# Kernel optimization log

Hardware: AMD Instinct MI355X
Metric: run time of the kernel (lower is better)

Reference implementation:

```python
import jax, jax.numpy as jnp
import numpy as np

E = 8          # node_emb_dim (number of LSTM ensembles)
H = 128        # fixed_lstm_hidden
D = 8          # feature dim
CONT = 168     # cont_len (encoder length)
HORIZON = 24   # decoder length
T = CONT + HORIZON
B = 4096       # batch of node ids
NUM_TS = 4096


def _lstm(xs, W, U, b, h0, c0):
    """Time-major LSTM (Keras gate order i,f,g,o). xs: [T,B,in]. Returns final (h,c) and all hs."""
    def step(carry, x):
        h, c = carry
        z = x @ W + h @ U + b                      # [B, 4H]
        i, f, g, o = jnp.split(z, 4, axis=-1)
        i = jax.nn.sigmoid(i)
        f = jax.nn.sigmoid(f)
        g = jnp.tanh(g)
        o = jax.nn.sigmoid(o)
        c = f * c + i * g
        h = o * jnp.tanh(c)
        return (h, c), h
    (h, c), hs = jax.lax.scan(step, (h0, c0), xs)
    return h, c, hs


def setup_inputs() -> dict:
    key = jax.random.key(0)
    ks = jax.random.split(key, 12)
    s = 0.05  # small init scale to keep LSTM gates unsaturated
    return {
        "feats": jax.random.normal(ks[0], (T, D), jnp.float32),
        "y_prev": jax.random.normal(ks[1], (CONT, B), jnp.float32),
        "nid": jax.random.randint(ks[2], (B,), 0, NUM_TS, jnp.int32),
        "emb_table": jax.random.uniform(ks[3], (NUM_TS, E), jnp.float32),
        "enc_W": jax.random.normal(ks[4], (E, 1 + D, 4 * H), jnp.float32) * s,
        "enc_U": jax.random.normal(ks[5], (E, H, 4 * H), jnp.float32) * s,
        "enc_b": jnp.zeros((E, 4 * H), jnp.float32),
        "dec_W": jax.random.normal(ks[6], (E, D, 4 * H), jnp.float32) * s,
        "dec_U": jax.random.normal(ks[7], (E, H, 4 * H), jnp.float32) * s,
        "dec_b": jnp.zeros((E, 4 * H), jnp.float32),
        "out_w": jax.random.normal(ks[8], (E, H), jnp.float32) * s,
    }


def reference(feats, y_prev, nid, emb_table, enc_W, enc_U, enc_b, dec_W, dec_U, dec_b, out_w):
    cont_len = y_prev.shape[0]
    b = nid.shape[0]
    # normalized node embedding: abs then row-normalize, then lookup
    embs = jnp.abs(emb_table)
    embs = embs / jnp.sum(embs, axis=1, keepdims=True)
    node_emb = embs[nid]                                   # [B, E]
    # broadcast features over batch (time-major)
    feats_b = jnp.broadcast_to(feats[:, None, :], (feats.shape[0], b, feats.shape[1]))
    enc_inp = jnp.concatenate([y_prev[..., None], feats_b[:cont_len]], axis=-1)  # [CONT,B,1+D]
    feats_futr = feats_b[cont_len:]                        # [HOR,B,D]
    hdim = enc_U.shape[1]
    h0 = jnp.zeros((b, hdim), feats.dtype)
    c0 = jnp.zeros((b, hdim), feats.dtype)

    def run_one(eW, eU, eb, dW, dU, db, ow):
        h, c, _ = _lstm(enc_inp, eW, eU, eb, h0, c0)
        _, _, hs = _lstm(feats_futr, dW, dU, db, h, c)     # [HOR,B,H]
        return jnp.einsum('tbh,h->tb', hs, ow)             # Dense(1, no bias) -> [HOR,B]

    outs = jax.vmap(run_one)(enc_W, enc_U, enc_b, dec_W, dec_U, dec_b, out_w)  # [E,HOR,B]
    fixed_effect = jnp.einsum('etb,be->tb', outs, node_emb)                    # [HOR,B]
    return fixed_effect
```

## Files before the change

### kernel.cpp

```cpp
#include <hip/hip_runtime.h>
#include <stdint.h>
#include <type_traits>

#define NE 8
#define NH 128
#define ND 8
#define NCONT 168
#define NHOR 24
#define NB 4096
#define NG 512
#define BT 64

typedef float f32x4 __attribute__((ext_vector_type(4)));
typedef short bf16x8 __attribute__((ext_vector_type(8)));
typedef unsigned int u32x2 __attribute__((ext_vector_type(2)));

__device__ __forceinline__ unsigned short f2bf(float f){
  union { float f; unsigned u; } v; v.f = f;
  unsigned r = (v.u + 0x7FFFu + ((v.u >> 16) & 1u)) >> 16;
  return (unsigned short)r;
}
__device__ __forceinline__ unsigned cvt_pk_bf16(float lo, float hi){
  unsigned r;
  asm("v_cvt_pk_bf16_f32 %0, %1, %2" : "=v"(r) : "v"(lo), "v"(hi));
  return r;
}
__device__ __forceinline__ float sigm(float x){
  return __builtin_amdgcn_rcpf(1.0f + __builtin_amdgcn_exp2f(-1.44269504f * x));
}
__device__ __forceinline__ float tanh_fast(float x){
  return 1.0f - 2.0f * __builtin_amdgcn_rcpf(1.0f + __builtin_amdgcn_exp2f(2.88539008f * x));
}

__global__ void prep_fxw_enc(const float* __restrict__ feats, const float* __restrict__ W,
                             const float* __restrict__ bias, float* __restrict__ out){
  int idx = blockIdx.x * blockDim.x + threadIdx.x;
  if (idx >= NE * NCONT * NG) return;
  int j = idx & (NG - 1);
  int t = (idx >> 9) % NCONT;
  int e = idx / (NCONT * NG);
  float s = bias[e * NG + j];
  #pragma unroll
  for (int i = 0; i < ND; ++i)
    s += feats[t * ND + i] * W[(e * 9 + 1 + i) * NG + j];
  out[idx] = s;
}

__global__ void prep_fxw_dec(const float* __restrict__ feats, const float* __restrict__ W,
                             const float* __restrict__ bias, float* __restrict__ out){
  int idx = blockIdx.x * blockDim.x + threadIdx.x;
  if (idx >= NE * NHOR * NG) return;
  int j = idx & (NG - 1);
  int t = (idx >> 9) % NHOR;
  int e = idx / (NHOR * NG);
  float s = bias[e * NG + j];
  #pragma unroll
  for (int i = 0; i < ND; ++i)
    s += feats[(NCONT + t) * ND + i] * W[(e * ND + i) * NG + j];
  out[idx] = s;
}

__global__ void prep_node(const int* __restrict__ nid, const float* __restrict__ emb,
                          float* __restrict__ node_w){
  int b = blockIdx.x * blockDim.x + threadIdx.x;
  if (b >= NB) return;
  int n = nid[b];
  float a[NE]; float s = 0.f;
  #pragma unroll
  for (int e = 0; e < NE; ++e){ a[e] = fabsf(emb[n * NE + e]); s += a[e]; }
  float inv = 1.0f / s;
  #pragma unroll
  for (int e = 0; e < NE; ++e) node_w[b * NE + e] = a[e] * inv;
}

__global__ __launch_bounds__(512, 2) void lstm_main(
    const float* __restrict__ y_prev,
    const float* __restrict__ enc_W,
    const float* __restrict__ enc_U,
    const float* __restrict__ dec_U,
    const float* __restrict__ out_w,
    const float* __restrict__ fxw_enc,
    const float* __restrict__ fxw_dec,
    float* __restrict__ ws_out)
{
  __shared__ unsigned short hl[2][BT * NH];
  __shared__ float part[2][BT][9];

  const int tid  = threadIdx.x;
  const int lane = tid & 63;
  const int w    = tid >> 6;
  const int e    = blockIdx.x & 7;
  const int b0   = (blockIdx.x >> 3) * BT;
  const int l15  = lane & 15;
  const int l4   = lane >> 4;
  const int hc0  = w * 16 + l4 * 4;

  const int q   = (l15 >> 2) & 1;
  const int Ae  = l15 * 128 + ((l4 ^ (l15 & 3)) << 3);
  const int rb0 = 2 * (Ae + q * 32);
  const int rb1 = 2 * (Ae + (1 - q) * 32);
  const int wb  = 2 * ((l15 * 128 + hc0) ^ ((l15 & 7) << 3));

  {
    f32x4 z4 = {0.f, 0.f, 0.f, 0.f};
    ((f32x4*)&hl[0][0])[tid]       = z4;
    ((f32x4*)&hl[0][0])[tid + 512] = z4;
  }

  bf16x8 ut[4][4];
  {
    const float* Ub = enc_U + e * NH * NG + w * 16 + l15;
    #pragma unroll
    for (int g = 0; g < 4; ++g)
      #pragma unroll
      for (int kc = 0; kc < 4; ++kc){
        const float* p = Ub + (kc * 32 + l4 * 8) * NG + g * NH;
        bf16x8 v;
        #pragma unroll
        for (int j = 0; j < 8; ++j) v[j] = (short)f2bf(p[j * NG]);
        ut[g][kc] = v;
      }
  }

  f32x4 w04[4];
  #pragma unroll
  for (int g = 0; g < 4; ++g)
    w04[g] = *(const f32x4*)&enc_W[(e * 9) * NG + g * NH + hc0];

  float cs[4][4];
  #pragma unroll
  for (int nf = 0; nf < 4; ++nf)
    #pragma unroll
    for (int rg = 0; rg < 4; ++rg) cs[nf][rg] = 0.f;

  const float* fxe = fxw_enc + e * NCONT * NG;
  const float* yp  = y_prev + b0;

  __syncthreads();

  auto step = [&](auto Bc, auto ENCc, const float* fxptr, float* pout){
    constexpr int  B   = decltype(Bc)::value;
    constexpr bool ENC = decltype(ENCc)::value;

    f32x4 fxv[4];
    #pragma unroll
    for (int g = 0; g < 4; ++g) fxv[g] = *(const f32x4*)&fxptr[g * NH + hc0];
    float yv[4];
    if (ENC){
      #pragma unroll
      for (int nf = 0; nf < 4; ++nf) yv[nf] = yp[nf * 16 + l15];
    }

    f32x4 acc[4][4];
    #pragma unroll
    for (int kc = 0; kc < 4; ++kc){
      bf16x8 hb[4];
      #pragma unroll
      for (int nf = 0; nf < 4; ++nf)
        hb[nf] = *(const bf16x8*)((const char*)hl +
                   (B * 16384 + nf * 4096 + (kc >> 1) * 128) + ((kc & 1) ? rb1 : rb0));
      #pragma unroll
      for (int nf = 0; nf < 4; ++nf)
        #pragma unroll
        for (int g = 0; g < 4; ++g){
          if (kc == 0)
            acc[nf][g] = __builtin_amdgcn_mfma_f32_16x16x32_bf16(ut[g][0], hb[nf], fxv[g], 0, 0, 0);
          else
            acc[nf][g] = __builtin_amdgcn_mfma_f32_16x16x32_bf16(ut[g][kc], hb[nf], acc[nf][g], 0, 0, 0);
        }
    }

    #pragma unroll
    for (int nf = 0; nf < 4; ++nf){
      float hh[4];
      #pragma unroll
      for (int rg = 0; rg < 4; ++rg){
        float zi = acc[nf][0][rg];
        float zf = acc[nf][1][rg];
        float zg = acc[nf][2][rg];
        float zo = acc[nf][3][rg];
        if (ENC){
          float y = yv[nf];
          zi += y * w04[0][rg]; zf += y * w04[1][rg];
          zg += y * w04[2][rg]; zo += y * w04[3][rg];
        }
        float gi = sigm(zi), gf = sigm(zf);
        float gg = tanh_fast(zg), go = sigm(zo);
        float c  = gf * cs[nf][rg] + gi * gg;
        cs[nf][rg] = c;
        hh[rg] = go * tanh_fast(c);
      }
      u32x2 pk;
      pk.x = cvt_pk_bf16(hh[0], hh[1]);
      pk.y = cvt_pk_bf16(hh[2], hh[3]);
      *(u32x2*)((char*)hl + ((B ^ 1) * 16384 + nf * 4096) + wb) = pk;
      if (!ENC) pout[nf] = hh[0]*pout[4] + hh[1]*pout[5] + hh[2]*pout[6] + hh[3]*pout[7];
    }
    __syncthreads();
  };

  for (int t = 0; t < NCONT; t += 2){
    step(std::integral_constant<int,0>{}, std::true_type{}, fxe, nullptr);
    fxe += NG; yp += NB;
    step(std::integral_constant<int,1>{}, std::true_type{}, fxe, nullptr);
    fxe += NG; yp += NB;
  }

  {
    const float* Ub = dec_U + e * NH * NG + w * 16 + l15;
    #pragma unroll
    for (int g = 0; g < 4; ++g)
      #pragma unroll
      for (int kc = 0; kc < 4; ++kc){
        const float* p = Ub + (kc * 32 + l4 * 8) * NG + g * NH;
        bf16x8 v;
        #pragma unroll
        for (int j = 0; j < 8; ++j) v[j] = (short)f2bf(p[j * NG]);
        ut[g][kc] = v;
      }
  }
  f32x4 ow4 = *(const f32x4*)&out_w[e * NH + hc0];

  const float* fxd = fxw_dec + e * NHOR * NG;

  #pragma unroll 1
  for (int td = 0; td < NHOR; td += 2){
    #pragma unroll
    for (int sub = 0; sub < 2; ++sub){
      float pbuf[8];
      pbuf[4] = ow4[0]; pbuf[5] = ow4[1]; pbuf[6] = ow4[2]; pbuf[7] = ow4[3];
      if (sub == 0)
        step(std::integral_constant<int,0>{}, std::false_type{}, fxd, pbuf);
      else
        step(std::integral_constant<int,1>{}, std::false_type{}, fxd, pbuf);
      fxd += NG;
      int t = td + sub;
      int pb = t & 1;
      #pragma unroll
      for (int nf = 0; nf < 4; ++nf){
        pbuf[nf] += __shfl_xor(pbuf[nf], 16);
        pbuf[nf] += __shfl_xor(pbuf[nf], 32);
      }
      if (lane < 16){
        #pragma unroll
        for (int nf = 0; nf < 4; ++nf) part[pb][nf * 16 + l15][w] = pbuf[nf];
      }
      __syncthreads();
      if (w == 0){
        float s = 0.f;
        #pragma unroll
        for (int ww = 0; ww < 8; ++ww) s += part[pb][lane][ww];
        ws_out[(e * NHOR + t) * NB + b0 + lane] = s;
      }
    }
  }
}

__global__ void finalize(const float* __restrict__ ws_out, const float* __restrict__ node_w,
                         float* __restrict__ out){
  int idx = blockIdx.x * blockDim.x + threadIdx.x;
  if (idx >= NHOR * NB) return;
  int b = idx & (NB - 1);
  float s = 0.f;
  #pragma unroll
  for (int e = 0; e < NE; ++e)
    s += ws_out[e * NHOR * NB + idx] * node_w[b * NE + e];
  out[idx] = s;
}

extern "C" void kernel_launch(void* const* d_in, const int* in_sizes, int n_in,
                              void* d_out, int out_size, void* d_ws, size_t ws_size,
                              hipStream_t stream) {
  const float* feats  = (const float*)d_in[0];
  const float* y_prev = (const float*)d_in[1];
  const int*   nid    = (const int*)  d_in[2];
  const float* emb    = (const float*)d_in[3];
  const float* enc_W  = (const float*)d_in[4];
  const float* enc_U  = (const float*)d_in[5];
  const float* enc_b  = (const float*)d_in[6];
  const float* dec_W  = (const float*)d_in[7];
  const float* dec_U  = (const float*)d_in[8];
  const float* dec_b  = (const float*)d_in[9];
  const float* out_w  = (const float*)d_in[10];
  float* out = (float*)d_out;

  float* ws      = (float*)d_ws;
  float* fxw_enc = ws;
  float* fxw_dec = fxw_enc + NE * NCONT * NG;
  float* node_w  = fxw_dec + NE * NHOR * NG;
  float* ws_out  = node_w + NB * NE;

  prep_fxw_enc<<<(NE * NCONT * NG + 255) / 256, 256, 0, stream>>>(feats, enc_W, enc_b, fxw_enc);
  prep_fxw_dec<<<(NE * NHOR * NG + 255) / 256, 256, 0, stream>>>(feats, dec_W, dec_b, fxw_dec);
  prep_node<<<(NB + 255) / 256, 256, 0, stream>>>(nid, emb, node_w);
  lstm_main<<<NE * (NB / BT), 512, 0, stream>>>(y_prev, enc_W, enc_U, dec_U, out_w,
                                                fxw_enc, fxw_dec, ws_out);
  finalize<<<(NHOR * NB + 255) / 256, 256, 0, stream>>>(ws_out, node_w, out);
}
```

Measured before the change: 1.290 ms.

## Use packed rational-polynomial sigmoid/tanh and prefetch next-step gate inputs

Replaces the exp2+rcp sigmoid and tanh with clamped rational polynomial approximations on float2 vectors, sharing one reciprocal across each pair. The intent is to cut transcendental-unit work and allow packed FMA in the LSTM gate epilogue. It also prefetches the next timestep's fx bias and y_prev values during the MFMA phase to hide global load latency. The cost is many more FMA instructions per element, extra registers for the prefetched values, and a small loss of accuracy near the clamp bounds.

```diff
diff --git a/kernel.cpp b/kernel.cpp
--- a/kernel.cpp
+++ b/kernel.cpp
@@ -12,6 +12,7 @@
 #define BT 64
 
 typedef float f32x4 __attribute__((ext_vector_type(4)));
+typedef float f32x2 __attribute__((ext_vector_type(2)));
 typedef short bf16x8 __attribute__((ext_vector_type(8)));
 typedef unsigned int u32x2 __attribute__((ext_vector_type(2)));
 
@@ -25,11 +26,53 @@
   asm("v_cvt_pk_bf16_f32 %0, %1, %2" : "=v"(r) : "v"(lo), "v"(hi));
   return r;
 }
-__device__ __forceinline__ float sigm(float x){
-  return __builtin_amdgcn_rcpf(1.0f + __builtin_amdgcn_exp2f(-1.44269504f * x));
-}
-__device__ __forceinline__ float tanh_fast(float x){
-  return 1.0f - 2.0f * __builtin_amdgcn_rcpf(1.0f + __builtin_amdgcn_exp2f(2.88539008f * x));
+
+__device__ __forceinline__ f32x2 splat2(float v){ f32x2 r; r.x = v; r.y = v; return r; }
+__device__ __forceinline__ f32x2 lo2(f32x4 v){ return __builtin_shufflevector(v, v, 0, 1); }
+__device__ __forceinline__ f32x2 hi2(f32x4 v){ return __builtin_shufflevector(v, v, 2, 3); }
+__device__ __forceinline__ f32x2 fma2(f32x2 a, f32x2 b, f32x2 c){
+  return __builtin_elementwise_fma(a, b, c);
+}
+__device__ __forceinline__ f32x2 med2(f32x2 x, float lo, float hi){
+  f32x2 o;
+  o.x = __builtin_amdgcn_fmed3f(x.x, lo, hi);
+  o.y = __builtin_amdgcn_fmed3f(x.y, lo, hi);
+  return o;
+}
+__device__ __forceinline__ f32x2 inv2(f32x2 q){
+  float pr = q.x * q.y;
+  float r  = __builtin_amdgcn_rcpf(pr);
+  f32x2 o; o.x = r * q.y; o.y = r * q.x; return o;
+}
+
+__device__ __forceinline__ f32x2 tanh2(f32x2 x){
+  x = med2(x, -7.90531110763549805f, 7.90531110763549805f);
+  f32x2 t = x * x;
+  f32x2 p = fma2(t, splat2(-2.76076847742355e-16f), splat2(2.00018790482477e-13f));
+  p = fma2(p, t, splat2(-8.60467152213735e-11f));
+  p = fma2(p, t, splat2(5.12229709037114e-08f));
+  p = fma2(p, t, splat2(1.48572235717979e-05f));
+  p = fma2(p, t, splat2(6.37261928875436e-04f));
+  p = fma2(p, t, splat2(4.89352455891786e-03f));
+  f32x2 q = fma2(t, splat2(1.19825839466702e-06f), splat2(1.18534705686654e-04f));
+  q = fma2(q, t, splat2(2.26843463243900e-03f));
+  q = fma2(q, t, splat2(4.89352518554385e-03f));
+  return (x * p) * inv2(q);
+}
+
+__device__ __forceinline__ f32x2 sigm2(f32x2 x){
+  x = med2(x, -15.8106222152709961f, 15.8106222152709961f);
+  f32x2 t = x * x;
+  f32x2 p = fma2(t, splat2(-1.68503935489719e-20f), splat2(4.88327125201360e-17f));
+  p = fma2(p, t, splat2(-8.40299953333725e-14f));
+  p = fma2(p, t, splat2(2.00089730170748e-10f));
+  p = fma2(p, t, splat2(2.32144118309342e-07f));
+  p = fma2(p, t, splat2(3.98288705547148e-05f));
+  p = fma2(p, t, splat2(1.22338113972947e-03f));
+  f32x2 q = fma2(t, splat2(1.87227874166722e-08f), splat2(7.40841910541588e-06f));
+  q = fma2(q, t, splat2(5.67108658109750e-04f));
+  q = fma2(q, t, splat2(4.89352518554385e-03f));
+  return fma2(x * p, inv2(q), splat2(0.5f));
 }
 
 __global__ void prep_fxw_enc(const float* __restrict__ feats, const float* __restrict__ W,
@@ -122,33 +165,39 @@
       }
   }
 
-  f32x4 w04[4];
-  #pragma unroll
-  for (int g = 0; g < 4; ++g)
-    w04[g] = *(const f32x4*)&enc_W[(e * 9) * NG + g * NH + hc0];
-
-  float cs[4][4];
-  #pragma unroll
-  for (int nf = 0; nf < 4; ++nf)
-    #pragma unroll
-    for (int rg = 0; rg < 4; ++rg) cs[nf][rg] = 0.f;
+  f32x2 w042[4][2];
+  #pragma unroll
+  for (int g = 0; g < 4; ++g){
+    f32x4 t4 = *(const f32x4*)&enc_W[(e * 9) * NG + g * NH + hc0];
+    w042[g][0] = lo2(t4); w042[g][1] = hi2(t4);
+  }
+
+  f32x2 cs2[4][2];
+  #pragma unroll
+  for (int nf = 0; nf < 4; ++nf){ cs2[nf][0] = splat2(0.f); cs2[nf][1] = splat2(0.f); }
+
+  f32x2 ow2[2];
+  f32x4 fxv[4];
+  float yv[4];
 
   const float* fxe = fxw_enc + e * NCONT * NG;
   const float* yp  = y_prev + b0;
 
+  #pragma unroll
+  for (int g = 0; g < 4; ++g) fxv[g] = *(const f32x4*)&fxe[g * NH + hc0];
+  #pragma unroll
+  for (int nf = 0; nf < 4; ++nf) yv[nf] = yp[nf * 16 + l15];
+
   __syncthreads();
 
-  auto step = [&](auto Bc, auto ENCc, const float* fxptr, float* pout){
+  auto step = [&](auto Bc, auto ENCc, const float* fxn, const float* ypn, float* pout){
     constexpr int  B   = decltype(Bc)::value;
     constexpr bool ENC = decltype(ENCc)::value;
 
-    f32x4 fxv[4];
-    #pragma unroll
-    for (int g = 0; g < 4; ++g) fxv[g] = *(const f32x4*)&fxptr[g * NH + hc0];
-    float yv[4];
-    if (ENC){
-      #pragma unroll
-      for (int nf = 0; nf < 4; ++nf) yv[nf] = yp[nf * 16 + l15];
+    float ycur[4];
+    if constexpr (ENC){
+      #pragma unroll
+      for (int nf = 0; nf < 4; ++nf) ycur[nf] = yv[nf];
     }
 
     f32x4 acc[4][4];
@@ -171,39 +220,52 @@
     }
 
     #pragma unroll
+    for (int g = 0; g < 4; ++g) fxv[g] = *(const f32x4*)&fxn[g * NH + hc0];
+    if constexpr (ENC){
+      #pragma unroll
+      for (int nf = 0; nf < 4; ++nf) yv[nf] = ypn[nf * 16 + l15];
+    }
+
+    #pragma unroll
     for (int nf = 0; nf < 4; ++nf){
-      float hh[4];
-      #pragma unroll
-      for (int rg = 0; rg < 4; ++rg){
-        float zi = acc[nf][0][rg];
-        float zf = acc[nf][1][rg];
-        float zg = acc[nf][2][rg];
-        float zo = acc[nf][3][rg];
-        if (ENC){
-          float y = yv[nf];
-          zi += y * w04[0][rg]; zf += y * w04[1][rg];
-          zg += y * w04[2][rg]; zo += y * w04[3][rg];
+      f32x2 h2[2];
+      #pragma unroll
+      for (int hf = 0; hf < 2; ++hf){
+        f32x2 zi = hf ? hi2(acc[nf][0]) : lo2(acc[nf][0]);
+        f32x2 zf = hf ? hi2(acc[nf][1]) : lo2(acc[nf][1]);
+        f32x2 zg = hf ? hi2(acc[nf][2]) : lo2(acc[nf][2]);
+        f32x2 zo = hf ? hi2(acc[nf][3]) : lo2(acc[nf][3]);
+        if constexpr (ENC){
+          f32x2 y2 = splat2(ycur[nf]);
+          zi = fma2(y2, w042[0][hf], zi);
+          zf = fma2(y2, w042[1][hf], zf);
+          zg = fma2(y2, w042[2][hf], zg);
+          zo = fma2(y2, w042[3][hf], zo);
         }
-        float gi = sigm(zi), gf = sigm(zf);
-        float gg = tanh_fast(zg), go = sigm(zo);
-        float c  = gf * cs[nf][rg] + gi * gg;
-        cs[nf][rg] = c;
-        hh[rg] = go * tanh_fast(c);
+        f32x2 gi = sigm2(zi), gf = sigm2(zf);
+        f32x2 gg = tanh2(zg), go = sigm2(zo);
+        f32x2 c  = fma2(gf, cs2[nf][hf], gi * gg);
+        cs2[nf][hf] = c;
+        h2[hf] = go * tanh2(c);
       }
       u32x2 pk;
-      pk.x = cvt_pk_bf16(hh[0], hh[1]);
-      pk.y = cvt_pk_bf16(hh[2], hh[3]);
+      pk.x = cvt_pk_bf16(h2[0].x, h2[0].y);
+      pk.y = cvt_pk_bf16(h2[1].x, h2[1].y);
       *(u32x2*)((char*)hl + ((B ^ 1) * 16384 + nf * 4096) + wb) = pk;
-      if (!ENC) pout[nf] = hh[0]*pout[4] + hh[1]*pout[5] + hh[2]*pout[6] + hh[3]*pout[7];
+      if constexpr (!ENC){
+        f32x2 pp = fma2(h2[0], ow2[0], h2[1] * ow2[1]);
+        pout[nf] = pp.x + pp.y;
+      }
     }
     __syncthreads();
   };
 
   for (int t = 0; t < NCONT; t += 2){
-    step(std::integral_constant<int,0>{}, std::true_type{}, fxe, nullptr);
-    fxe += NG; yp += NB;
-    step(std::integral_constant<int,1>{}, std::true_type{}, fxe, nullptr);
-    fxe += NG; yp += NB;
+    step(std::integral_constant<int,0>{}, std::true_type{}, fxe + NG, yp + NB, nullptr);
+    const float* fx2 = (t + 2 < NCONT) ? fxe + 2 * NG : fxe;
+    const float* yp2 = (t + 2 < NCONT) ? yp + 2 * NB  : yp;
+    step(std::integral_constant<int,1>{}, std::true_type{}, fx2, yp2, nullptr);
+    fxe += 2 * NG; yp += 2 * NB;
   }
 
   {
@@ -219,40 +281,44 @@
         ut[g][kc] = v;
       }
   }
-  f32x4 ow4 = *(const f32x4*)&out_w[e * NH + hc0];
+  {
+    f32x4 ow4 = *(const f32x4*)&out_w[e * NH + hc0];
+    ow2[0] = lo2(ow4); ow2[1] = hi2(ow4);
+  }
 
   const float* fxd = fxw_dec + e * NHOR * NG;
+  #pragma unroll
+  for (int g = 0; g < 4; ++g) fxv[g] = *(const f32x4*)&fxd[g * NH + hc0];
+
+  auto emit = [&](int t, float* pbuf){
+    #pragma unroll
+    for (int nf = 0; nf < 4; ++nf){
+      pbuf[nf] += __shfl_xor(pbuf[nf], 16);
+      pbuf[nf] += __shfl_xor(pbuf[nf], 32);
+    }
+    int pb = t & 1;
+    if (lane < 16){
+      #pragma unroll
+      for (int nf = 0; nf < 4; ++nf) part[pb][nf * 16 + l15][w] = pbuf[nf];
+    }
+    __syncthreads();
+    if (w == 0){
+      float s = 0.f;
+      #pragma unroll
+      for (int ww = 0; ww < 8; ++ww) s += part[pb][lane][ww];
+      ws_out[(e * NHOR + t) * NB + b0 + lane] = s;
+    }
+  };
 
   #pragma unroll 1
   for (int td = 0; td < NHOR; td += 2){
-    #pragma unroll
-    for (int sub = 0; sub < 2; ++sub){
-      float pbuf[8];
-      pbuf[4] = ow4[0]; pbuf[5] = ow4[1]; pbuf[6] = ow4[2]; pbuf[7] = ow4[3];
-      if (sub == 0)
-        step(std::integral_constant<int,0>{}, std::false_type{}, fxd, pbuf);
-      else
-        step(std::integral_constant<int,1>{}, std::false_type{}, fxd, pbuf);
-      fxd += NG;
-      int t = td + sub;
-      int pb = t & 1;
-      #pragma unroll
-      for (int nf = 0; nf < 4; ++nf){
-        pbuf[nf] += __shfl_xor(pbuf[nf], 16);
-        pbuf[nf] += __shfl_xor(pbuf[nf], 32);
-      }
-      if (lane < 16){
-        #pragma unroll
-        for (int nf = 0; nf < 4; ++nf) part[pb][nf * 16 + l15][w] = pbuf[nf];
-      }
-      __syncthreads();
-      if (w == 0){
-        float s = 0.f;
-        #pragma unroll
-        for (int ww = 0; ww < 8; ++ww) s += part[pb][lane][ww];
-        ws_out[(e * NHOR + t) * NB + b0 + lane] = s;
-      }
-    }
+    float pbuf[4];
+    step(std::integral_constant<int,0>{}, std::false_type{}, fxd + NG, nullptr, pbuf);
+    emit(td, pbuf);
+    const float* fx2 = (td + 2 < NHOR) ? fxd + 2 * NG : fxd;
+    step(std::integral_constant<int,1>{}, std::false_type{}, fx2, nullptr, pbuf);
+    emit(td + 1, pbuf);
+    fxd += 2 * NG;
   }
 }
 
```

Result: slower. 1.703 ms (+32.0%).
